# Performance work log

Hardware: AMD Instinct MI355X
Metric: run time of the kernel (lower is better)

The kernel has to match this reference:

```python
import jax, jax.numpy as jnp
import numpy as np

SEQ = 2048
DIM = 4096
N_HEADS = 32
N_KV_HEADS = 8
HEAD_DIM = DIM // N_HEADS  # 128
ROPE_THETA = 500000.0


def setup_inputs() -> dict:
    key = jax.random.key(0)
    ks = jax.random.split(key, 5)
    s = 0.02  # keep activations numerically tame
    return {
        "x": jax.random.normal(ks[0], (SEQ, DIM), dtype=jnp.float32),
        "wq": jax.random.normal(ks[1], (DIM, DIM), dtype=jnp.float32) * s,
        "wk": jax.random.normal(ks[2], (N_KV_HEADS * HEAD_DIM, DIM), dtype=jnp.float32) * s,
        "wv": jax.random.normal(ks[3], (N_KV_HEADS * HEAD_DIM, DIM), dtype=jnp.float32) * s,
        "wo": jax.random.normal(ks[4], (DIM, DIM), dtype=jnp.float32) * s,
    }


def _rope(t):
    # t: [S, H, D]; pairs (t[...,2i], t[...,2i+1]) rotated by angle pos * theta^(-i/(D/2)),
    # matching torch.view_as_complex on x.view(S, -1, 2) * polar(1, pos*freq).
    S, H, D = t.shape
    half = D // 2
    freqs = 1.0 / (ROPE_THETA ** (jnp.arange(half, dtype=jnp.float32) / half))
    ang = jnp.arange(S, dtype=jnp.float32)[:, None] * freqs[None, :]  # [S, half]
    cos = jnp.cos(ang)[:, None, :]  # [S, 1, half]
    sin = jnp.sin(ang)[:, None, :]
    tr = t.reshape(S, H, half, 2)
    x0, x1 = tr[..., 0], tr[..., 1]
    r0 = x0 * cos - x1 * sin
    r1 = x0 * sin + x1 * cos
    return jnp.stack([r0, r1], axis=-1).reshape(S, H, D)


def reference(x, wq, wk, wv, wo):
    S = x.shape[0]
    group = N_HEADS // N_KV_HEADS
    # Per-head projections (batched over heads instead of python loop)
    q = jnp.einsum("sd,hkd->shk", x, wq.reshape(N_HEADS, HEAD_DIM, DIM))        # [S,H,D]
    k = jnp.einsum("sd,hkd->shk", x, wk.reshape(N_KV_HEADS, HEAD_DIM, DIM))     # [S,Hkv,D]
    v = jnp.einsum("sd,hkd->shk", x, wv.reshape(N_KV_HEADS, HEAD_DIM, DIM))     # [S,Hkv,D]
    q = _rope(q)
    k = _rope(k)
    # GQA: q head h uses kv head h // group -> repeat kv heads consecutively
    kf = jnp.repeat(k, group, axis=1)  # [S,H,D]
    vf = jnp.repeat(v, group, axis=1)  # [S,H,D]
    scores = jnp.einsum("shd,thd->hst", q, kf) / jnp.sqrt(jnp.float32(HEAD_DIM))
    causal = jnp.tril(jnp.ones((S, S), dtype=bool))
    scores = jnp.where(causal[None], scores, -jnp.inf)
    probs = jax.nn.softmax(scores, axis=-1)
    out = jnp.einsum("hst,thd->shd", probs, vf).reshape(S, N_HEADS * HEAD_DIM)
    return out @ wo.T
```

## Files before the change

### kernel.cpp

```cpp
#include <hip/hip_runtime.h>
#include <stdint.h>
#include <math.h>

#define SEQ   2048
#define DIM   4096
#define NHEAD 32
#define NKV   8
#define HD    128
#define KVDIM (NKV*HD)

typedef __bf16 bf16x8 __attribute__((ext_vector_type(8)));
typedef float  f32x4  __attribute__((ext_vector_type(4)));

__device__ __forceinline__ uint16_t f2bf(float f) {
  uint32_t u = __float_as_uint(f);
  uint32_t r = (u + 0x7FFFu + ((u >> 16) & 1u)) >> 16;
  return (uint16_t)r;
}
__device__ __forceinline__ bf16x8 ld_frag(const uint16_t* p) {
  return *(const bf16x8*)p;
}
__device__ __forceinline__ void async_cp16(const void* g, void* lds) {
  __builtin_amdgcn_global_load_lds(
      (const __attribute__((address_space(1))) void*)g,
      (__attribute__((address_space(3))) void*)lds, 16, 0, 0);
}
__device__ __forceinline__ uint32_t lds_u32(const void* p) {
  return (uint32_t)(uintptr_t)(const __attribute__((address_space(3))) void*)p;
}
__device__ __forceinline__ bf16x8 ds_read_b128a(uint32_t addr) {
  f32x4 r;
  asm volatile("ds_read_b128 %0, %1" : "=v"(r) : "v"(addr));
  return __builtin_bit_cast(bf16x8, r);
}

__global__ __launch_bounds__(256) void k_conv_all(
    const float* __restrict__ x, const float* __restrict__ wq,
    const float* __restrict__ wk, const float* __restrict__ wv,
    uint16_t* __restrict__ xb, uint16_t* __restrict__ wqkvb) {
  size_t i = (size_t)blockIdx.x * 256 + threadIdx.x;
  const float* s; uint16_t* d; size_t off;
  if (i < 2097152)      { s = x;  d = xb;                 off = i; }
  else if (i < 6291456) { s = wq; d = wqkvb;              off = i - 2097152; }
  else if (i < 7340032) { s = wk; d = wqkvb + 16777216u;  off = i - 6291456; }
  else                  { s = wv; d = wqkvb + 20971520u;  off = i - 7340032; }
  const float4 v = ((const float4*)s)[off];
  ushort4 o;
  o.x = f2bf(v.x); o.y = f2bf(v.y); o.z = f2bf(v.z); o.w = f2bf(v.w);
  ((ushort4*)d)[off] = o;
}

__global__ __launch_bounds__(256) void k_conv(const float* __restrict__ s,
                                              uint16_t* __restrict__ d, int n4) {
  int i = blockIdx.x * 256 + threadIdx.x;
  if (i >= n4) return;
  const float4 v = ((const float4*)s)[i];
  ushort4 o;
  o.x = f2bf(v.x); o.y = f2bf(v.y); o.z = f2bf(v.z); o.w = f2bf(v.w);
  ((ushort4*)d)[i] = o;
}

#define G256_TB   8192

#define G256_PROLOGUE(Aptr, Bptr)                                               \
  __shared__ __align__(16) uint16_t sA[4 * G256_TB];                            \
  __shared__ __align__(16) uint16_t sB[4 * G256_TB];                            \
  const int tid  = threadIdx.x;                                                 \
  const int lane = tid & 63;                                                    \
  const int wv   = tid >> 6;                                                    \
  const int quad = lane >> 4;                                                   \
  const int l16  = lane & 15;                                                   \
  const int wm   = (wv >> 2) << 7;                                \
  const int wn   = (wv & 3) << 6;                             \
  const uint16_t* gA = Aptr + (size_t)m0 * DIM;                                 \
  const uint16_t* gB = Bptr + (size_t)n0 * DIM;                                 \
  const int srow0 = tid >> 2;                                                   \
  const int sc0   = (tid & 3) ^ ((srow0 >> 1) & 3);                             \
  const int srow1 = (512 + tid) >> 2;                                           \
  const int sc1   = (tid & 3) ^ ((srow1 >> 1) & 3);                             \
  const size_t sga0 = (size_t)srow0 * DIM + sc0 * 8;                            \
  const size_t sga1 = (size_t)srow1 * DIM + sc1 * 8;                            \
  const uint32_t sAb = lds_u32(sA);                                             \
  const uint32_t sBb = lds_u32(sB);                                             \
  uint32_t offA[8], offB[4];                                                    \
  _Pragma("unroll")                                                             \
  for (int t = 0; t < 8; t++) {                                                 \
    int r_ = wm + t * 16 + l16;                                                 \
    offA[t] = (uint32_t)((r_ * 32 + (quad ^ ((r_ >> 1) & 3)) * 8) * 2);         \
  }                                                                             \
  _Pragma("unroll")                                                             \
  for (int t = 0; t < 4; t++) {                                                 \
    int r_ = wn + t * 16 + l16;                                                 \
    offB[t] = (uint32_t)((r_ * 32 + (quad ^ ((r_ >> 1) & 3)) * 8) * 2);         \
  }                                                                             \
  f32x4 acc[8][4] = {};                                                         \
                                             \
  async_cp16(gA + sga0,      sA + tid * 8);                                     \
  async_cp16(gB + sga0,      sB + tid * 8);                                     \
  async_cp16(gA + sga1,      sA + 4096 + tid * 8);                              \
  async_cp16(gB + sga1,      sB + 4096 + tid * 8);                              \
  async_cp16(gA + sga0 + 32, sA + G256_TB + tid * 8);                           \
  async_cp16(gB + sga0 + 32, sB + G256_TB + tid * 8);                           \
  async_cp16(gA + sga1 + 32, sA + G256_TB + 4096 + tid * 8);                    \
  async_cp16(gB + sga1 + 32, sB + G256_TB + 4096 + tid * 8);                    \
  asm volatile("s_waitcnt vmcnt(4)" ::: "memory");            \
  __builtin_amdgcn_s_barrier();                                                 \
  for (int T = 0; T < 128; T++) {                                               \
    const uint32_t cbB  = (uint32_t)((T & 3) * (G256_TB * 2));                  \
    const uint32_t aBse = sAb + cbB;                                            \
    const uint32_t bBse = sBb + cbB;                                            \
    const int  k2 = (T + 2) * 32;                                               \
    const bool pf = (T + 2 < 128);                                              \
    const int  db = ((T + 2) & 3) * G256_TB;                                    \
              \
    bf16x8 af0[4], bfv[4];                                                      \
    _Pragma("unroll")                                                           \
    for (int t = 0; t < 4; t++) {                                               \
      af0[t] = ds_read_b128a(aBse + offA[t]);                                   \
      bfv[t] = ds_read_b128a(bBse + offB[t]);                                   \
    }                                                                           \
    if (pf) {                                                                   \
      async_cp16(gA + sga0 + k2, sA + db + tid * 8);                            \
      async_cp16(gB + sga0 + k2, sB + db + tid * 8);                            \
    }                                                                           \
    __builtin_amdgcn_s_barrier();                                               \
    asm volatile("s_waitcnt lgkmcnt(0)" ::: "memory");                          \
    __builtin_amdgcn_sched_barrier(0);                                          \
    __builtin_amdgcn_s_setprio(1);                                              \
    _Pragma("unroll")                                                           \
    for (int mt = 0; mt < 4; mt++)                                              \
      _Pragma("unroll")                                                         \
      for (int nt = 0; nt < 4; nt++)                                            \
        acc[mt][nt] = __builtin_amdgcn_mfma_f32_16x16x32_bf16(af0[mt], bfv[nt], \
                                                              acc[mt][nt], 0, 0, 0); \
    __builtin_amdgcn_s_setprio(0);                                              \
    __builtin_amdgcn_s_barrier();                                               \
              \
    bf16x8 af1[4];                                                              \
    _Pragma("unroll")                                                           \
    for (int t = 0; t < 4; t++)                                                 \
      af1[t] = ds_read_b128a(aBse + offA[4 + t]);                               \
    if (pf) {                                                                   \
      async_cp16(gA + sga1 + k2, sA + db + 4096 + tid * 8);                     \
      async_cp16(gB + sga1 + k2, sB + db + 4096 + tid * 8);                     \
    }                                                                           \
    __builtin_amdgcn_s_barrier();                                               \
    asm volatile("s_waitcnt lgkmcnt(0)" ::: "memory");                          \
    __builtin_amdgcn_sched_barrier(0);                                          \
    __builtin_amdgcn_s_setprio(1);                                              \
    _Pragma("unroll")                                                           \
    for (int mt = 0; mt < 4; mt++)                                              \
      _Pragma("unroll")                                                         \
      for (int nt = 0; nt < 4; nt++)                                            \
        acc[4 + mt][nt] = __builtin_amdgcn_mfma_f32_16x16x32_bf16(af1[mt], bfv[nt], \
                                                                  acc[4 + mt][nt], 0, 0, 0); \
    __builtin_amdgcn_s_setprio(0);                                              \
          \
    if (pf) { asm volatile("s_waitcnt vmcnt(4)" ::: "memory"); }                \
    else    { asm volatile("s_waitcnt vmcnt(0)" ::: "memory"); }                \
    __builtin_amdgcn_s_barrier();                                               \
  }

__global__ __launch_bounds__(512, 2) void k_gemm_qkv(
    const uint16_t* __restrict__ xb, const uint16_t* __restrict__ wqkvb,
    uint16_t* __restrict__ Qb, uint16_t* __restrict__ Kb, uint16_t* __restrict__ Vb)
{
  const int bx = blockIdx.x;
  const int m0 = blockIdx.y * 256;
  const int n0 = bx * 256;
  G256_PROLOGUE(xb, wqkvb)

  const int region = (bx < 16) ? 0 : (bx < 20 ? 1 : 2);
  uint16_t* outp; int ldC, cbase;
  if (region == 0)      { outp = Qb; ldC = DIM;   cbase = n0; }
  else if (region == 1) { outp = Kb; ldC = KVDIM; cbase = n0 - 4096; }
  else                  { outp = Vb; ldC = KVDIM; cbase = n0 - 5120; }

  #pragma unroll
  for (int mt = 0; mt < 8; mt++)
    #pragma unroll
    for (int nt = 0; nt < 4; nt++) {
      const int col = cbase + wn + nt * 16 + l16;
      const int d = col & 127;
      const float freq = expf(-0.20503693f * (float)(d >> 1));
      const float sgn = (d & 1) ? 1.0f : -1.0f;
      #pragma unroll
      for (int r = 0; r < 4; r++) {
        const int row = m0 + wm + mt * 16 + quad * 4 + r;
        float v = acc[mt][nt][r];
        if (region < 2) {
          float p = __shfl_xor(v, 1, 64);
          float ang = (float)row * freq;
          float sn, cs;
          sincosf(ang, &sn, &cs);
          v = v * cs + p * sn * sgn;
        }
        outp[(size_t)row * ldC + col] = f2bf(v);
      }
    }
}

__global__ __launch_bounds__(512, 2) void k_gemm_o(
    const uint16_t* __restrict__ ab, const uint16_t* __restrict__ wob,
    float* __restrict__ out)
{
  const int m0 = blockIdx.y * 256;
  const int n0 = blockIdx.x * 256;
  G256_PROLOGUE(ab, wob)
  #pragma unroll
  for (int mt = 0; mt < 8; mt++)
    #pragma unroll
    for (int nt = 0; nt < 4; nt++)
      #pragma unroll
      for (int r = 0; r < 4; r++) {
        int row = m0 + wm + mt * 16 + quad * 4 + r;
        int col = n0 + wn + nt * 16 + l16;
        out[(size_t)row * DIM + col] = acc[mt][nt][r];
      }
}

__global__ __launch_bounds__(256) void k_vtrans(const uint16_t* __restrict__ Vb,
                                                uint16_t* __restrict__ VT) {
  __shared__ uint16_t t[64][72];
  const int s0 = blockIdx.x * 64;
  const int c0 = blockIdx.y * 64;
  const int tid = threadIdx.x;
  #pragma unroll
  for (int i = 0; i < 2; i++) {
    int idx = i * 256 + tid;
    int r = idx >> 3, ch = idx & 7;
    uint4 dv = *(const uint4*)(Vb + (size_t)(s0 + r) * KVDIM + c0 + ch * 8);
    *(uint4*)(&t[r][ch * 8]) = dv;
  }
  __syncthreads();
  const int kvh = c0 >> 7;
  const int dbase = c0 & 127;
  #pragma unroll
  for (int i = 0; i < 2; i++) {
    int idx = i * 256 + tid;
    int d = idx >> 3, sc = idx & 7;
    uint16_t tmp[8];
    #pragma unroll
    for (int j2 = 0; j2 < 8; j2++) tmp[j2] = t[sc * 8 + j2][d];
    *(uint4*)(VT + (size_t)kvh * HD * SEQ + (size_t)(dbase + d) * SEQ + s0 + sc * 8) = *(const uint4*)tmp;
  }
}

#define BKV 64
#define NPAIR 40
__device__ __constant__ uint8_t c_pair[NPAIR] = {
  12,16,20,24,28,29,32,33,36,37,40,41,44,45,46,48,49,50,52,53,54,56,57,58,60,61,62,63,
  8,25,42,59,
  4,21,38,55,
  0,17,34,51
};
__device__ __constant__ uint8_t c_base[16] = {0,1,2,3,4,6,8,10,12,15,18,21,24,28,32,36};

__global__ __launch_bounds__(256) void k_flash_split(
    const uint16_t* __restrict__ Qb, const uint16_t* __restrict__ Kb,
    const uint16_t* __restrict__ VT, uint16_t* __restrict__ Opart,
    float* __restrict__ ml)
{
  const int pair = c_pair[blockIdx.x];
  const int qt   = pair >> 2;
  const int seg  = pair & 3;
  const int h    = blockIdx.y;
  const int kvh  = h >> 2;
  const int slot = h * NPAIR + c_base[qt] + seg;
  const int tid  = threadIdx.x;
  const int lane = tid & 63;
  const int wv   = tid >> 6;
  const int quad = lane >> 4;
  const int l16  = lane & 15;
  const int q0   = qt * 128;

  __shared__ __align__(16) uint16_t sK[BKV * 128];
  __shared__ __align__(16) uint16_t sVT[HD * BKV];
  __shared__ __align__(16) uint16_t sP[4 * 32 * 72];

  const uint16_t* Kbase  = Kb + kvh * HD;
  const uint16_t* VTbase = VT + (size_t)kvh * HD * SEQ;

  bf16x8 qf[2][4];
  #pragma unroll
  for (int mt = 0; mt < 2; mt++)
    #pragma unroll
    for (int ks = 0; ks < 4; ks++)
      qf[mt][ks] = ld_frag(Qb + (size_t)(q0 + wv * 32 + mt * 16 + l16) * DIM + h * HD + ks * 32 + quad * 8);

  __align__(16) uint16_t ones_bits[8];
  #pragma unroll
  for (int j = 0; j < 8; j++) ones_bits[j] = (l16 == 0) ? 0x3F80 : 0;
  const bf16x8 onesf = *(const bf16x8*)ones_bits;

  f32x4 Oacc[2][8] = {};
  f32x4 Lacc[2] = {};

  const float scale = 0.08838834764831845f;
  const float MFIX = 12.0f;
  const int j0 = seg * 8;
  const int j1 = min(j0 + 8, 2 * (qt + 1));

  for (int j = j0; j < j1; j++) {
    const int t0 = j * BKV;
    #pragma unroll
    for (int i = 0; i < 4; i++) {
      int pos = i * 256 + tid;
      int row = pos >> 4, g = (pos & 15) ^ (row & 7);
      async_cp16(Kbase + (size_t)(t0 + row) * KVDIM + g * 8, sK + pos * 8);
      int vrow = pos >> 3, vg = (pos & 7) ^ (vrow & 7);
      async_cp16(VTbase + (size_t)vrow * SEQ + t0 + vg * 8, sVT + pos * 8);
    }
    __syncthreads();

    bool active = (t0 <= q0 + wv * 32 + 31);
    if (active) {
      f32x4 Sacc[2][4] = {};
      #pragma unroll
      for (int ks = 0; ks < 4; ks++) {
        bf16x8 kf[4];
        #pragma unroll
        for (int nt = 0; nt < 4; nt++)
          kf[nt] = ld_frag(sK + (nt * 16 + l16) * 128 + (((ks * 4 + quad) ^ (l16 & 7)) * 8));
        #pragma unroll
        for (int mt = 0; mt < 2; mt++)
          #pragma unroll
          for (int nt = 0; nt < 4; nt++)
            Sacc[mt][nt] = __builtin_amdgcn_mfma_f32_16x16x32_bf16(qf[mt][ks], kf[nt], Sacc[mt][nt], 0, 0, 0);
      }
      const bool diag = (t0 + BKV - 1) > (q0 + wv * 32);
      #pragma unroll
      for (int mt = 0; mt < 2; mt++)
        #pragma unroll
        for (int nt = 0; nt < 4; nt++)
          #pragma unroll
          for (int r = 0; r < 4; r++) {
            float sv = Sacc[mt][nt][r] * scale - MFIX;
            bool msk = false;
            if (diag) {
              int qg = q0 + wv * 32 + mt * 16 + quad * 4 + r;
              int tg = t0 + nt * 16 + l16;
              msk = tg > qg;
            }
            float pv = msk ? 0.0f : __expf(sv);
            sP[(wv * 32 + mt * 16 + quad * 4 + r) * 72 + nt * 16 + l16] = f2bf(pv);
          }
      #pragma unroll
      for (int ks = 0; ks < 2; ks++) {
        bf16x8 pf[2], vf[8];
        #pragma unroll
        for (int mt = 0; mt < 2; mt++)
          pf[mt] = ld_frag(sP + (wv * 32 + mt * 16 + l16) * 72 + ks * 32 + quad * 8);
        #pragma unroll
        for (int dt = 0; dt < 8; dt++)
          vf[dt] = ld_frag(sVT + (dt * 16 + l16) * 64 + (((ks * 4 + quad) ^ (l16 & 7)) * 8));
        #pragma unroll
        for (int mt = 0; mt < 2; mt++) {
          Lacc[mt] = __builtin_amdgcn_mfma_f32_16x16x32_bf16(pf[mt], onesf, Lacc[mt], 0, 0, 0);
          #pragma unroll
          for (int dt = 0; dt < 8; dt++)
            Oacc[mt][dt] = __builtin_amdgcn_mfma_f32_16x16x32_bf16(pf[mt], vf[dt], Oacc[mt][dt], 0, 0, 0);
        }
      }
    }
    __syncthreads();
  }

  uint16_t* Op = Opart + (size_t)slot * (128 * 128);
  #pragma unroll
  for (int mt = 0; mt < 2; mt++)
    #pragma unroll
    for (int r = 0; r < 4; r++) {
      int row = wv * 32 + mt * 16 + quad * 4 + r;
      #pragma unroll
      for (int dt = 0; dt < 8; dt++)
        Op[row * 128 + dt * 16 + l16] = f2bf(Oacc[mt][dt][r]);
      if (l16 == 0)
        ml[(size_t)slot * 128 + row] = Lacc[mt][r];
    }
}

__global__ __launch_bounds__(256) void k_combine(
    const uint16_t* __restrict__ Opart, const float* __restrict__ ml,
    uint16_t* __restrict__ attnb)
{
  const int qt = blockIdx.x;
  const int h  = blockIdx.y;
  const int nseg = (qt >> 2) + 1;
  const int slot0 = h * NPAIR + c_base[qt];
  const int tid = threadIdx.x;
  const int row = tid >> 1;
  const int dh  = (tid & 1) * 64;

  float L = 0.0f;
  #pragma unroll
  for (int i = 0; i < 4; i++)
    if (i < nseg) L += ml[(size_t)(slot0 + i) * 128 + row];
  const float invL = 1.0f / L;

  uint16_t* dst = attnb + (size_t)(qt * 128 + row) * DIM + h * HD + dh;
  #pragma unroll
  for (int c = 0; c < 8; c++) {
    int d = dh + c * 8;
    float acc[8] = {};
    #pragma unroll
    for (int i = 0; i < 4; i++) {
      if (i < nseg) {
        bf16x8 v = ld_frag(Opart + (size_t)(slot0 + i) * (128 * 128) + row * 128 + d);
        #pragma unroll
        for (int j = 0; j < 8; j++) acc[j] += (float)v[j];
      }
    }
    uint16_t outv[8];
    #pragma unroll
    for (int j = 0; j < 8; j++) outv[j] = f2bf(acc[j] * invL);
    *(uint4*)(dst + c * 8) = *(const uint4*)outv;
  }
}

extern "C" void kernel_launch(void* const* d_in, const int* in_sizes, int n_in,
                              void* d_out, int out_size, void* d_ws, size_t ws_size,
                              hipStream_t stream) {
  const float* x  = (const float*)d_in[0];
  const float* wq = (const float*)d_in[1];
  const float* wk = (const float*)d_in[2];
  const float* wv = (const float*)d_in[3];
  const float* wo = (const float*)d_in[4];
  float* out = (float*)d_out;

  uint8_t* ws = (uint8_t*)d_ws;
  uint16_t* xb     = (uint16_t*)(ws + 0);
  uint16_t* wqkvb  = (uint16_t*)(ws + 16777216ull);
  uint16_t* Qb     = (uint16_t*)(ws + 67108864ull);
  uint16_t* Kb     = (uint16_t*)(ws + 83886080ull);
  uint16_t* Vb     = (uint16_t*)(ws + 88080384ull);
  uint16_t* VT     = (uint16_t*)(ws + 16777216ull);
  uint16_t* Opart  = (uint16_t*)(ws + 20971520ull);
  float*    mlbuf  = (float*)   (ws + 62914560ull);
  uint16_t* wob    = (uint16_t*)(ws + 16777216ull);
  uint16_t* attnb  = xb;

  k_conv_all<<<32768, 256, 0, stream>>>(x, wq, wk, wv, xb, wqkvb);
  k_gemm_qkv<<<dim3(24, 8), 512, 0, stream>>>(xb, wqkvb, Qb, Kb, Vb);
  k_vtrans<<<dim3(32, 16), 256, 0, stream>>>(Vb, VT);
  k_flash_split<<<dim3(NPAIR, 32), 256, 0, stream>>>(Qb, Kb, VT, Opart, mlbuf);
  k_combine<<<dim3(16, 32), 256, 0, stream>>>(Opart, mlbuf, attnb);
  k_conv<<<16384, 256, 0, stream>>>(wo, wob, 4194304);
  k_gemm_o<<<dim3(16, 8), 512, 0, stream>>>(attnb, wob, out);
}
```

Baseline: 613.5 us.

## Restructure GEMM mainloop to K=64 double-buffered tiles with quadrant-split staging

Replaces the 4-stage K=32 LDS ring in the shared 256x256 GEMM prologue with a 2-stage K=64 double buffer. Each iteration is split into four quadrant MFMA phases, and each phase issues one half-tile global-to-LDS stage for the next K step. It also changes the LDS swizzle to an 8-chunk XOR layout and remaps which accumulators the epilogues read. The aim is fewer barriers per unit of K and better overlap of loads with MFMA. The cost is more complex waitcnt and barrier ordering that must stay correct.

```diff
diff --git a/kernel.cpp b/kernel.cpp
--- a/kernel.cpp
+++ b/kernel.cpp
@@ -60,11 +60,17 @@
   ((ushort4*)d)[i] = o;
 }
 
-#define G256_TB   8192
+
+#define STG2(gX, sX, row1g, halfel, Tn) do {                                    \
+    async_cp16(gX + (size_t)(row1g) * DIM + (size_t)(Tn) * 64 + cchunk * 8,     \
+               sX + (halfel) + (row1g) * 64 + (tid & 7) * 8);                   \
+    async_cp16(gX + (size_t)((row1g) + 128) * DIM + (size_t)(Tn) * 64 + cchunk * 8, \
+               sX + (halfel) + ((row1g) + 128) * 64 + (tid & 7) * 8);           \
+  } while (0)
 
 #define G256_PROLOGUE(Aptr, Bptr)                                               \
-  __shared__ __align__(16) uint16_t sA[4 * G256_TB];                            \
-  __shared__ __align__(16) uint16_t sB[4 * G256_TB];                            \
+  __shared__ __align__(16) uint16_t sA[2 * 16384];                              \
+  __shared__ __align__(16) uint16_t sB[2 * 16384];                              \
   const int tid  = threadIdx.x;                                                 \
   const int lane = tid & 63;                                                    \
   const int wv   = tid >> 6;                                                    \
@@ -74,92 +80,119 @@
   const int wn   = (wv & 3) << 6;                             \
   const uint16_t* gA = Aptr + (size_t)m0 * DIM;                                 \
   const uint16_t* gB = Bptr + (size_t)n0 * DIM;                                 \
-  const int srow0 = tid >> 2;                                                   \
-  const int sc0   = (tid & 3) ^ ((srow0 >> 1) & 3);                             \
-  const int srow1 = (512 + tid) >> 2;                                           \
-  const int sc1   = (tid & 3) ^ ((srow1 >> 1) & 3);                             \
-  const size_t sga0 = (size_t)srow0 * DIM + sc0 * 8;                            \
-  const size_t sga1 = (size_t)srow1 * DIM + sc1 * 8;                            \
+  const int crow   = tid >> 3;                                                  \
+  const int cchunk = (tid & 7) ^ (crow & 7);                                    \
+  const int rA0 = crow;                                   \
+  const int rA1 = crow + 64;                              \
+  const int rB0 = ((crow >> 5) << 6) + (crow & 31);       \
+  const int rB1 = rB0 + 32;                               \
   const uint32_t sAb = lds_u32(sA);                                             \
   const uint32_t sBb = lds_u32(sB);                                             \
-  uint32_t offA[8], offB[4];                                                    \
+  uint32_t rowbA[4], rowbB[2], colb[2];                                         \
   _Pragma("unroll")                                                             \
-  for (int t = 0; t < 8; t++) {                                                 \
-    int r_ = wm + t * 16 + l16;                                                 \
-    offA[t] = (uint32_t)((r_ * 32 + (quad ^ ((r_ >> 1) & 3)) * 8) * 2);         \
-  }                                                                             \
+  for (int t = 0; t < 4; t++) rowbA[t] = (uint32_t)((wm + t * 16 + l16) * 128); \
   _Pragma("unroll")                                                             \
-  for (int t = 0; t < 4; t++) {                                                 \
-    int r_ = wn + t * 16 + l16;                                                 \
-    offB[t] = (uint32_t)((r_ * 32 + (quad ^ ((r_ >> 1) & 3)) * 8) * 2);         \
-  }                                                                             \
+  for (int u = 0; u < 2; u++) rowbB[u] = (uint32_t)((wn + u * 16 + l16) * 128); \
+  _Pragma("unroll")                                                             \
+  for (int ks = 0; ks < 2; ks++)                                                \
+    colb[ks] = (uint32_t)((((ks * 4 + quad) ^ (l16 & 7)) * 16));                \
   f32x4 acc[8][4] = {};                                                         \
-                                             \
-  async_cp16(gA + sga0,      sA + tid * 8);                                     \
-  async_cp16(gB + sga0,      sB + tid * 8);                                     \
-  async_cp16(gA + sga1,      sA + 4096 + tid * 8);                              \
-  async_cp16(gB + sga1,      sB + 4096 + tid * 8);                              \
-  async_cp16(gA + sga0 + 32, sA + G256_TB + tid * 8);                           \
-  async_cp16(gB + sga0 + 32, sB + G256_TB + tid * 8);                           \
-  async_cp16(gA + sga1 + 32, sA + G256_TB + 4096 + tid * 8);                    \
-  async_cp16(gB + sga1 + 32, sB + G256_TB + 4096 + tid * 8);                    \
-  asm volatile("s_waitcnt vmcnt(4)" ::: "memory");            \
+  bf16x8 af[4][2], bf0[2][2], bf1[2][2];                                        \
+            \
+  STG2(gA, sA, rA0, 0, 0);                                                      \
+  STG2(gB, sB, rB0, 0, 0);                                                      \
+  STG2(gB, sB, rB1, 0, 0);                                                      \
+  STG2(gA, sA, rA1, 0, 0);                                                      \
+  asm volatile("s_waitcnt vmcnt(4)" ::: "memory");      \
   __builtin_amdgcn_s_barrier();                                                 \
-  for (int T = 0; T < 128; T++) {                                               \
-    const uint32_t cbB  = (uint32_t)((T & 3) * (G256_TB * 2));                  \
-    const uint32_t aBse = sAb + cbB;                                            \
-    const uint32_t bBse = sBb + cbB;                                            \
-    const int  k2 = (T + 2) * 32;                                               \
-    const bool pf = (T + 2 < 128);                                              \
-    const int  db = ((T + 2) & 3) * G256_TB;                                    \
-              \
-    bf16x8 af0[4], bfv[4];                                                      \
+  for (int T = 0; T < 64; T++) {                                                \
+    const uint32_t dsel   = (uint32_t)((T & 1) << 15);     \
+    const int      halfel = ((T + 1) & 1) << 14;          \
+    const int      Tn     = T + 1;                                              \
+     \
     _Pragma("unroll")                                                           \
     for (int t = 0; t < 4; t++) {                                               \
-      af0[t] = ds_read_b128a(aBse + offA[t]);                                   \
-      bfv[t] = ds_read_b128a(bBse + offB[t]);                                   \
+      af[t][0] = ds_read_b128a(sAb + dsel + rowbA[t] + colb[0]);                \
+      af[t][1] = ds_read_b128a(sAb + dsel + rowbA[t] + colb[1]);                \
     }                                                                           \
-    if (pf) {                                                                   \
-      async_cp16(gA + sga0 + k2, sA + db + tid * 8);                            \
-      async_cp16(gB + sga0 + k2, sB + db + tid * 8);                            \
+    _Pragma("unroll")                                                           \
+    for (int u = 0; u < 2; u++) {                                               \
+      bf0[u][0] = ds_read_b128a(sBb + dsel + rowbB[u] + colb[0]);               \
+      bf0[u][1] = ds_read_b128a(sBb + dsel + rowbB[u] + colb[1]);               \
     }                                                                           \
+    STG2(gA, sA, rA0, halfel, Tn);                                              \
     __builtin_amdgcn_s_barrier();                                               \
     asm volatile("s_waitcnt lgkmcnt(0)" ::: "memory");                          \
     __builtin_amdgcn_sched_barrier(0);                                          \
     __builtin_amdgcn_s_setprio(1);                                              \
     _Pragma("unroll")                                                           \
-    for (int mt = 0; mt < 4; mt++)                                              \
+    for (int ks = 0; ks < 2; ks++)                                              \
       _Pragma("unroll")                                                         \
-      for (int nt = 0; nt < 4; nt++)                                            \
-        acc[mt][nt] = __builtin_amdgcn_mfma_f32_16x16x32_bf16(af0[mt], bfv[nt], \
-                                                              acc[mt][nt], 0, 0, 0); \
+      for (int t = 0; t < 4; t++)                                               \
+        _Pragma("unroll")                                                       \
+        for (int u = 0; u < 2; u++)                                             \
+          acc[t][u] = __builtin_amdgcn_mfma_f32_16x16x32_bf16(af[t][ks], bf0[u][ks], acc[t][u], 0, 0, 0); \
     __builtin_amdgcn_s_setprio(0);                                              \
+    asm volatile("s_waitcnt vmcnt(4)" ::: "memory");           \
     __builtin_amdgcn_s_barrier();                                               \
               \
-    bf16x8 af1[4];                                                              \
-    _Pragma("unroll")                                                           \
-    for (int t = 0; t < 4; t++)                                                 \
-      af1[t] = ds_read_b128a(aBse + offA[4 + t]);                               \
-    if (pf) {                                                                   \
-      async_cp16(gA + sga1 + k2, sA + db + 4096 + tid * 8);                     \
-      async_cp16(gB + sga1 + k2, sB + db + 4096 + tid * 8);                     \
+    _Pragma("unroll")                                                           \
+    for (int u = 0; u < 2; u++) {                                               \
+      bf1[u][0] = ds_read_b128a(sBb + dsel + 4096 + rowbB[u] + colb[0]);        \
+      bf1[u][1] = ds_read_b128a(sBb + dsel + 4096 + rowbB[u] + colb[1]);        \
     }                                                                           \
+    STG2(gB, sB, rB0, halfel, Tn);                                              \
     __builtin_amdgcn_s_barrier();                                               \
     asm volatile("s_waitcnt lgkmcnt(0)" ::: "memory");                          \
     __builtin_amdgcn_sched_barrier(0);                                          \
     __builtin_amdgcn_s_setprio(1);                                              \
     _Pragma("unroll")                                                           \
-    for (int mt = 0; mt < 4; mt++)                                              \
+    for (int ks = 0; ks < 2; ks++)                                              \
       _Pragma("unroll")                                                         \
-      for (int nt = 0; nt < 4; nt++)                                            \
-        acc[4 + mt][nt] = __builtin_amdgcn_mfma_f32_16x16x32_bf16(af1[mt], bfv[nt], \
-                                                                  acc[4 + mt][nt], 0, 0, 0); \
+      for (int t = 0; t < 4; t++)                                               \
+        _Pragma("unroll")                                                       \
+        for (int u = 0; u < 2; u++)                                             \
+          acc[t][2 + u] = __builtin_amdgcn_mfma_f32_16x16x32_bf16(af[t][ks], bf1[u][ks], acc[t][2 + u], 0, 0, 0); \
     __builtin_amdgcn_s_setprio(0);                                              \
-          \
-    if (pf) { asm volatile("s_waitcnt vmcnt(4)" ::: "memory"); }                \
-    else    { asm volatile("s_waitcnt vmcnt(0)" ::: "memory"); }                \
-    __builtin_amdgcn_s_barrier();                                               \
-  }
+    asm volatile("s_waitcnt vmcnt(4)" ::: "memory");          \
+    __builtin_amdgcn_s_barrier();                                               \
+             \
+    _Pragma("unroll")                                                           \
+    for (int t = 0; t < 4; t++) {                                               \
+      af[t][0] = ds_read_b128a(sAb + dsel + 8192 + rowbA[t] + colb[0]);         \
+      af[t][1] = ds_read_b128a(sAb + dsel + 8192 + rowbA[t] + colb[1]);         \
+    }                                                                           \
+    STG2(gB, sB, rB1, halfel, Tn);                                              \
+    __builtin_amdgcn_s_barrier();                                               \
+    asm volatile("s_waitcnt lgkmcnt(0)" ::: "memory");                          \
+    __builtin_amdgcn_sched_barrier(0);                                          \
+    __builtin_amdgcn_s_setprio(1);                                              \
+    _Pragma("unroll")                                                           \
+    for (int ks = 0; ks < 2; ks++)                                              \
+      _Pragma("unroll")                                                         \
+      for (int t = 0; t < 4; t++)                                               \
+        _Pragma("unroll")                                                       \
+        for (int u = 0; u < 2; u++)                                             \
+          acc[4 + t][u] = __builtin_amdgcn_mfma_f32_16x16x32_bf16(af[t][ks], bf0[u][ks], acc[4 + t][u], 0, 0, 0); \
+    __builtin_amdgcn_s_setprio(0);                                              \
+    __builtin_amdgcn_s_barrier();                                               \
+              \
+    STG2(gA, sA, rA1, halfel, Tn);                                              \
+    __builtin_amdgcn_s_barrier();                                               \
+    __builtin_amdgcn_sched_barrier(0);                                          \
+    __builtin_amdgcn_s_setprio(1);                                              \
+    _Pragma("unroll")                                                           \
+    for (int ks = 0; ks < 2; ks++)                                              \
+      _Pragma("unroll")                                                         \
+      for (int t = 0; t < 4; t++)                                               \
+        _Pragma("unroll")                                                       \
+        for (int u = 0; u < 2; u++)                                             \
+          acc[4 + t][2 + u] = __builtin_amdgcn_mfma_f32_16x16x32_bf16(af[t][ks], bf1[u][ks], acc[4 + t][2 + u], 0, 0, 0); \
+    __builtin_amdgcn_s_setprio(0);                                              \
+    asm volatile("s_waitcnt vmcnt(4)" ::: "memory");         \
+    __builtin_amdgcn_s_barrier();                                               \
+  }                                                                             \
+  asm volatile("s_waitcnt vmcnt(0)" ::: "memory");
 
 __global__ __launch_bounds__(512, 2) void k_gemm_qkv(
     const uint16_t* __restrict__ xb, const uint16_t* __restrict__ wqkvb,
@@ -177,27 +210,31 @@
   else                  { outp = Vb; ldC = KVDIM; cbase = n0 - 5120; }
 
   #pragma unroll
-  for (int mt = 0; mt < 8; mt++)
-    #pragma unroll
-    for (int nt = 0; nt < 4; nt++) {
-      const int col = cbase + wn + nt * 16 + l16;
-      const int d = col & 127;
-      const float freq = expf(-0.20503693f * (float)(d >> 1));
-      const float sgn = (d & 1) ? 1.0f : -1.0f;
-      #pragma unroll
-      for (int r = 0; r < 4; r++) {
-        const int row = m0 + wm + mt * 16 + quad * 4 + r;
-        float v = acc[mt][nt][r];
-        if (region < 2) {
-          float p = __shfl_xor(v, 1, 64);
-          float ang = (float)row * freq;
-          float sn, cs;
-          sincosf(ang, &sn, &cs);
-          v = v * cs + p * sn * sgn;
+  for (int mh = 0; mh < 2; mh++)
+    #pragma unroll
+    for (int t = 0; t < 4; t++)
+      #pragma unroll
+      for (int nh = 0; nh < 2; nh++)
+        #pragma unroll
+        for (int u = 0; u < 2; u++) {
+          const int col = cbase + wn + nh * 32 + u * 16 + l16;
+          const int d = col & 127;
+          const float freq = expf(-0.20503693f * (float)(d >> 1));
+          const float sgn = (d & 1) ? 1.0f : -1.0f;
+          #pragma unroll
+          for (int r = 0; r < 4; r++) {
+            const int row = m0 + wm + mh * 64 + t * 16 + quad * 4 + r;
+            float v = acc[mh * 4 + t][nh * 2 + u][r];
+            if (region < 2) {
+              float p = __shfl_xor(v, 1, 64);
+              float ang = (float)row * freq;
+              float sn, cs;
+              sincosf(ang, &sn, &cs);
+              v = v * cs + p * sn * sgn;
+            }
+            outp[(size_t)row * ldC + col] = f2bf(v);
+          }
         }
-        outp[(size_t)row * ldC + col] = f2bf(v);
-      }
-    }
 }
 
 __global__ __launch_bounds__(512, 2) void k_gemm_o(
@@ -208,15 +245,19 @@
   const int n0 = blockIdx.x * 256;
   G256_PROLOGUE(ab, wob)
   #pragma unroll
-  for (int mt = 0; mt < 8; mt++)
-    #pragma unroll
-    for (int nt = 0; nt < 4; nt++)
-      #pragma unroll
-      for (int r = 0; r < 4; r++) {
-        int row = m0 + wm + mt * 16 + quad * 4 + r;
-        int col = n0 + wn + nt * 16 + l16;
-        out[(size_t)row * DIM + col] = acc[mt][nt][r];
-      }
+  for (int mh = 0; mh < 2; mh++)
+    #pragma unroll
+    for (int t = 0; t < 4; t++)
+      #pragma unroll
+      for (int nh = 0; nh < 2; nh++)
+        #pragma unroll
+        for (int u = 0; u < 2; u++)
+          #pragma unroll
+          for (int r = 0; r < 4; r++) {
+            int row = m0 + wm + mh * 64 + t * 16 + quad * 4 + r;
+            int col = n0 + wn + nh * 32 + u * 16 + l16;
+            out[(size_t)row * DIM + col] = acc[mh * 4 + t][nh * 2 + u][r];
+          }
 }
 
 __global__ __launch_bounds__(256) void k_vtrans(const uint16_t* __restrict__ Vb,
```

Result: no change. 608.0 us (-0.9%).

## Restructure GEMM main loop with register double-buffered fragments and deeper prefetch

Applied to the files above, without the earlier changes.

Rewrites the shared 256x256 GEMM main loop used by the QKV and output projections. Each iteration now issues the LDS reads for the next k-step into a second fragment set while MFMAs consume the current one, prefetches three stages ahead instead of two, and uses one barrier per k-step instead of four. The aim is to hide LDS latency behind MFMA work and cut synchronisation overhead. The cost is higher register pressure from holding two full fragment sets at 512 threads, which risks spills.

```diff
diff --git a/kernel.cpp b/kernel.cpp
--- a/kernel.cpp
+++ b/kernel.cpp
@@ -60,11 +60,55 @@
   ((ushort4*)d)[i] = o;
 }
 
-#define G256_TB   8192
+
+#define STG32(Tn) do {                                                          \
+    const int _rg = ((Tn) & 3) * 8192;                                          \
+    async_cp16(gA + (size_t)crow * DIM + (size_t)(Tn) * 32 + cs * 8,            \
+               sA + _rg + tid * 8);                                             \
+    async_cp16(gA + (size_t)(crow + 128) * DIM + (size_t)(Tn) * 32 + cs * 8,    \
+               sA + _rg + 4096 + tid * 8);                                      \
+    async_cp16(gB + (size_t)crow * DIM + (size_t)(Tn) * 32 + cs * 8,            \
+               sB + _rg + tid * 8);                                             \
+    async_cp16(gB + (size_t)(crow + 128) * DIM + (size_t)(Tn) * 32 + cs * 8,    \
+               sB + _rg + 4096 + tid * 8);                                      \
+  } while (0)
+
+#define READ12(AF, BF, ringoff) do {                                            \
+    _Pragma("unroll")                                                           \
+    for (int _t = 0; _t < 8; _t++) AF[_t] = ds_read_b128a(offA[_t] + (ringoff));\
+    _Pragma("unroll")                                                           \
+    for (int _u = 0; _u < 4; _u++) BF[_u] = ds_read_b128a(offB[_u] + (ringoff));\
+  } while (0)
+
+#define MFMA32(AF, BF)                                                          \
+    _Pragma("unroll")                                                           \
+    for (int _t = 0; _t < 8; _t++)                                              \
+      _Pragma("unroll")                                                         \
+      for (int _u = 0; _u < 4; _u++)                                            \
+        acc[_t][_u] = __builtin_amdgcn_mfma_f32_16x16x32_bf16(AF[_t], BF[_u],   \
+                                                              acc[_t][_u], 0, 0, 0);
+
+#define BODY(CA, CB, NA, NB, T) do {                                            \
+    if ((T) + 3 < 128) STG32((T) + 3);                                          \
+    if ((T) + 1 < 128) {                                                        \
+      const uint32_t _ro = (uint32_t)((((T) + 1) & 3) << 14);                   \
+      READ12(NA, NB, _ro);                                                      \
+      asm volatile("s_waitcnt lgkmcnt(12)" ::: "memory");                       \
+    } else {                                                                    \
+      asm volatile("s_waitcnt lgkmcnt(0)" ::: "memory");                        \
+    }                                                                           \
+    __builtin_amdgcn_sched_barrier(0);                                          \
+    __builtin_amdgcn_s_setprio(1);                                              \
+    MFMA32(CA, CB);                                                             \
+    __builtin_amdgcn_s_setprio(0);                                              \
+    if ((T) + 3 < 128) { asm volatile("s_waitcnt vmcnt(4)" ::: "memory"); }     \
+    else               { asm volatile("s_waitcnt vmcnt(0)" ::: "memory"); }     \
+    if ((T) < 127) __builtin_amdgcn_s_barrier();                                \
+  } while (0)
 
 #define G256_PROLOGUE(Aptr, Bptr)                                               \
-  __shared__ __align__(16) uint16_t sA[4 * G256_TB];                            \
-  __shared__ __align__(16) uint16_t sB[4 * G256_TB];                            \
+  __shared__ __align__(16) uint16_t sA[4 * 8192];                               \
+  __shared__ __align__(16) uint16_t sB[4 * 8192];                               \
   const int tid  = threadIdx.x;                                                 \
   const int lane = tid & 63;                                                    \
   const int wv   = tid >> 6;                                                    \
@@ -74,91 +118,30 @@
   const int wn   = (wv & 3) << 6;                             \
   const uint16_t* gA = Aptr + (size_t)m0 * DIM;                                 \
   const uint16_t* gB = Bptr + (size_t)n0 * DIM;                                 \
-  const int srow0 = tid >> 2;                                                   \
-  const int sc0   = (tid & 3) ^ ((srow0 >> 1) & 3);                             \
-  const int srow1 = (512 + tid) >> 2;                                           \
-  const int sc1   = (tid & 3) ^ ((srow1 >> 1) & 3);                             \
-  const size_t sga0 = (size_t)srow0 * DIM + sc0 * 8;                            \
-  const size_t sga1 = (size_t)srow1 * DIM + sc1 * 8;                            \
+  const int crow = tid >> 2;                                                    \
+  const int cs   = (tid & 3) ^ ((crow >> 1) & 3);                               \
   const uint32_t sAb = lds_u32(sA);                                             \
   const uint32_t sBb = lds_u32(sB);                                             \
   uint32_t offA[8], offB[4];                                                    \
   _Pragma("unroll")                                                             \
   for (int t = 0; t < 8; t++) {                                                 \
     int r_ = wm + t * 16 + l16;                                                 \
-    offA[t] = (uint32_t)((r_ * 32 + (quad ^ ((r_ >> 1) & 3)) * 8) * 2);         \
+    offA[t] = sAb + (uint32_t)(r_ * 64 + (quad ^ ((r_ >> 1) & 3)) * 16);        \
   }                                                                             \
   _Pragma("unroll")                                                             \
-  for (int t = 0; t < 4; t++) {                                                 \
-    int r_ = wn + t * 16 + l16;                                                 \
-    offB[t] = (uint32_t)((r_ * 32 + (quad ^ ((r_ >> 1) & 3)) * 8) * 2);         \
+  for (int u = 0; u < 4; u++) {                                                 \
+    int r_ = wn + u * 16 + l16;                                                 \
+    offB[u] = sBb + (uint32_t)(r_ * 64 + (quad ^ ((r_ >> 1) & 3)) * 16);        \
   }                                                                             \
   f32x4 acc[8][4] = {};                                                         \
-                                             \
-  async_cp16(gA + sga0,      sA + tid * 8);                                     \
-  async_cp16(gB + sga0,      sB + tid * 8);                                     \
-  async_cp16(gA + sga1,      sA + 4096 + tid * 8);                              \
-  async_cp16(gB + sga1,      sB + 4096 + tid * 8);                              \
-  async_cp16(gA + sga0 + 32, sA + G256_TB + tid * 8);                           \
-  async_cp16(gB + sga0 + 32, sB + G256_TB + tid * 8);                           \
-  async_cp16(gA + sga1 + 32, sA + G256_TB + 4096 + tid * 8);                    \
-  async_cp16(gB + sga1 + 32, sB + G256_TB + 4096 + tid * 8);                    \
-  asm volatile("s_waitcnt vmcnt(4)" ::: "memory");            \
+  bf16x8 afC[8], bfC[4], afN[8], bfN[4];                                        \
+  STG32(0); STG32(1); STG32(2);                                                 \
+  asm volatile("s_waitcnt vmcnt(4)" ::: "memory");        \
   __builtin_amdgcn_s_barrier();                                                 \
-  for (int T = 0; T < 128; T++) {                                               \
-    const uint32_t cbB  = (uint32_t)((T & 3) * (G256_TB * 2));                  \
-    const uint32_t aBse = sAb + cbB;                                            \
-    const uint32_t bBse = sBb + cbB;                                            \
-    const int  k2 = (T + 2) * 32;                                               \
-    const bool pf = (T + 2 < 128);                                              \
-    const int  db = ((T + 2) & 3) * G256_TB;                                    \
-              \
-    bf16x8 af0[4], bfv[4];                                                      \
-    _Pragma("unroll")                                                           \
-    for (int t = 0; t < 4; t++) {                                               \
-      af0[t] = ds_read_b128a(aBse + offA[t]);                                   \
-      bfv[t] = ds_read_b128a(bBse + offB[t]);                                   \
-    }                                                                           \
-    if (pf) {                                                                   \
-      async_cp16(gA + sga0 + k2, sA + db + tid * 8);                            \
-      async_cp16(gB + sga0 + k2, sB + db + tid * 8);                            \
-    }                                                                           \
-    __builtin_amdgcn_s_barrier();                                               \
-    asm volatile("s_waitcnt lgkmcnt(0)" ::: "memory");                          \
-    __builtin_amdgcn_sched_barrier(0);                                          \
-    __builtin_amdgcn_s_setprio(1);                                              \
-    _Pragma("unroll")                                                           \
-    for (int mt = 0; mt < 4; mt++)                                              \
-      _Pragma("unroll")                                                         \
-      for (int nt = 0; nt < 4; nt++)                                            \
-        acc[mt][nt] = __builtin_amdgcn_mfma_f32_16x16x32_bf16(af0[mt], bfv[nt], \
-                                                              acc[mt][nt], 0, 0, 0); \
-    __builtin_amdgcn_s_setprio(0);                                              \
-    __builtin_amdgcn_s_barrier();                                               \
-              \
-    bf16x8 af1[4];                                                              \
-    _Pragma("unroll")                                                           \
-    for (int t = 0; t < 4; t++)                                                 \
-      af1[t] = ds_read_b128a(aBse + offA[4 + t]);                               \
-    if (pf) {                                                                   \
-      async_cp16(gA + sga1 + k2, sA + db + 4096 + tid * 8);                     \
-      async_cp16(gB + sga1 + k2, sB + db + 4096 + tid * 8);                     \
-    }                                                                           \
-    __builtin_amdgcn_s_barrier();                                               \
-    asm volatile("s_waitcnt lgkmcnt(0)" ::: "memory");                          \
-    __builtin_amdgcn_sched_barrier(0);                                          \
-    __builtin_amdgcn_s_setprio(1);                                              \
-    _Pragma("unroll")                                                           \
-    for (int mt = 0; mt < 4; mt++)                                              \
-      _Pragma("unroll")                                                         \
-      for (int nt = 0; nt < 4; nt++)                                            \
-        acc[4 + mt][nt] = __builtin_amdgcn_mfma_f32_16x16x32_bf16(af1[mt], bfv[nt], \
-                                                                  acc[4 + mt][nt], 0, 0, 0); \
-    __builtin_amdgcn_s_setprio(0);                                              \
-          \
-    if (pf) { asm volatile("s_waitcnt vmcnt(4)" ::: "memory"); }                \
-    else    { asm volatile("s_waitcnt vmcnt(0)" ::: "memory"); }                \
-    __builtin_amdgcn_s_barrier();                                               \
+  READ12(afC, bfC, 0u);                                                         \
+  for (int T = 0; T < 128; T += 2) {                                            \
+    BODY(afC, bfC, afN, bfN, T);                                                \
+    BODY(afN, bfN, afC, bfC, T + 1);                                            \
   }
 
 __global__ __launch_bounds__(512, 2) void k_gemm_qkv(
@@ -177,23 +160,23 @@
   else                  { outp = Vb; ldC = KVDIM; cbase = n0 - 5120; }
 
   #pragma unroll
-  for (int mt = 0; mt < 8; mt++)
-    #pragma unroll
-    for (int nt = 0; nt < 4; nt++) {
-      const int col = cbase + wn + nt * 16 + l16;
+  for (int t = 0; t < 8; t++)
+    #pragma unroll
+    for (int u = 0; u < 4; u++) {
+      const int col = cbase + wn + u * 16 + l16;
       const int d = col & 127;
       const float freq = expf(-0.20503693f * (float)(d >> 1));
       const float sgn = (d & 1) ? 1.0f : -1.0f;
       #pragma unroll
       for (int r = 0; r < 4; r++) {
-        const int row = m0 + wm + mt * 16 + quad * 4 + r;
-        float v = acc[mt][nt][r];
+        const int row = m0 + wm + t * 16 + quad * 4 + r;
+        float v = acc[t][u][r];
         if (region < 2) {
           float p = __shfl_xor(v, 1, 64);
           float ang = (float)row * freq;
-          float sn, cs;
-          sincosf(ang, &sn, &cs);
-          v = v * cs + p * sn * sgn;
+          float sn, cc2;
+          sincosf(ang, &sn, &cc2);
+          v = v * cc2 + p * sn * sgn;
         }
         outp[(size_t)row * ldC + col] = f2bf(v);
       }
@@ -208,14 +191,14 @@
   const int n0 = blockIdx.x * 256;
   G256_PROLOGUE(ab, wob)
   #pragma unroll
-  for (int mt = 0; mt < 8; mt++)
-    #pragma unroll
-    for (int nt = 0; nt < 4; nt++)
+  for (int t = 0; t < 8; t++)
+    #pragma unroll
+    for (int u = 0; u < 4; u++)
       #pragma unroll
       for (int r = 0; r < 4; r++) {
-        int row = m0 + wm + mt * 16 + quad * 4 + r;
-        int col = n0 + wn + nt * 16 + l16;
-        out[(size_t)row * DIM + col] = acc[mt][nt][r];
+        int row = m0 + wm + t * 16 + quad * 4 + r;
+        int col = n0 + wn + u * 16 + l16;
+        out[(size_t)row * DIM + col] = acc[t][u][r];
       }
 }
 
```

Result: no change. 611.5 us (-0.3%).
